# Performance work log

Measured on AMD Instinct MI355X. Metric: run time of the kernel, lower is better.

## Reference

```python
import jax, jax.numpy as jnp
import numpy as np

VOL = (32, 64, 64)          # 3D brain volume grid
B, N, D = 2, 4096, 1024     # batch, active voxels (seq_len), feature_dim
H, KNN = 16, 16             # num_heads, num_neighbors


def setup_inputs() -> dict:
    key = jax.random.key(0)
    k1, k2, k3, k4 = jax.random.split(key, 4)
    # boolean 3D mask with exactly N active voxels (so seq_len == #active)
    rng = np.random.default_rng(0)
    flat = np.zeros(int(np.prod(VOL)), dtype=bool)
    flat[rng.choice(flat.size, N, replace=False)] = True
    visual_cortex_mask = jnp.asarray(flat.reshape(VOL))
    x = jax.random.normal(k1, (B, N, D), dtype=jnp.float32)
    s = 1.0 / np.sqrt(D)
    Wq = jax.random.normal(k2, (D, D), dtype=jnp.float32) * s
    Wk = jax.random.normal(k3, (D, D), dtype=jnp.float32) * s
    Wv = jax.random.normal(k4, (D, D), dtype=jnp.float32) * s
    return {"x": x, "visual_cortex_mask": visual_cortex_mask,
            "Wq": Wq, "Wk": Wk, "Wv": Wv}


def reference(x, visual_cortex_mask, Wq, Wk, Wv):
    batch, seq_len, d = x.shape
    hd = d // H
    # --- kNN over active voxel coordinates (cdist + topk) ---
    flat = visual_cortex_mask.reshape(-1)
    (act,) = jnp.nonzero(flat, size=seq_len)  # flat indices of active voxels
    coords = jnp.stack(jnp.unravel_index(act, visual_cortex_mask.shape),
                       axis=1).astype(jnp.float32)           # [N, 3]
    sq = jnp.sum(coords * coords, axis=-1)                    # [N]
    d2 = sq[:, None] + sq[None, :] - 2.0 * (coords @ coords.T)  # squared dists
    _, nbr = jax.lax.top_k(-d2, KNN + 1)   # smallest distances first
    nbr = nbr[:, 1:]                       # drop self -> [N, KNN] positions
    # --- QKV projections (torch Linear: x @ W.T) ---
    q = (x @ Wq.T).reshape(batch, seq_len, H, hd)
    k = (x @ Wk.T).reshape(batch, seq_len, H, hd)
    v = (x @ Wv.T).reshape(batch, seq_len, H, hd)
    # --- gather-based sparse attention: each query attends only to its
    # KNN neighbors (exactly the block-mask semantics of the original) ---
    kn = k[:, nbr]   # [B, N, KNN, H, hd]
    vn = v[:, nbr]   # [B, N, KNN, H, hd]
    scale = 1.0 / np.sqrt(hd)
    scores = jnp.einsum('bnhd,bnkhd->bhnk', q, kn) * scale
    attn = jax.nn.softmax(scores, axis=-1)
    out = jnp.einsum('bhnk,bnkhd->bnhd', attn, vn).reshape(batch, seq_len, d)
    metric = k.mean(axis=2)  # key.mean over heads -> [B, N, hd]
    return out, metric
```

## Files before the change

kernel.cpp:

```cpp
#include <hip/hip_runtime.h>
#include <hip/hip_bf16.h>
#include <stdint.h>

#define BATCH 2
#define NPTS 4096
#define DMODEL 1024
#define NHEAD 16
#define HDIM 64
#define KNN 16
#define MASKN 131072
#define EBLK 128

typedef __attribute__((ext_vector_type(8))) short bf16x8;
typedef __attribute__((ext_vector_type(4))) float f32x4;

__device__ __forceinline__ float b2f(unsigned short u) {
    union { unsigned int i; float f; } c; c.i = ((unsigned int)u) << 16; return c.f;
}
__device__ __forceinline__ unsigned short f2b(float f) {
    unsigned int x = __float_as_uint(f);
    unsigned int r = (x + 0x7fffu + ((x >> 16) & 1u)) >> 16;
    return (unsigned short)r;
}
__device__ __forceinline__ unsigned int pack2f(float a, float b) {
    return (unsigned int)f2b(a) | ((unsigned int)f2b(b) << 16);
}
__device__ __forceinline__ void gload16(const unsigned short* g, unsigned short* l) {
    __builtin_amdgcn_global_load_lds((const __attribute__((address_space(1))) void*)g,
                                     (__attribute__((address_space(3))) void*)l, 16, 0, 0);
}

__global__ __launch_bounds__(256) void count8_kernel(const unsigned char* __restrict__ m8,
                                                     int* __restrict__ cnt8) {
    __shared__ int red[256];
    const int b = blockIdx.x, t = threadIdx.x;
    const uchar4 v = ((const uchar4*)m8)[b * 256 + t];
    red[t] = (v.x != 0) + (v.y != 0) + (v.z != 0) + (v.w != 0);
    __syncthreads();
    for (int off = 128; off >= 1; off >>= 1) {
        if (t < off) red[t] += red[t + off];
        __syncthreads();
    }
    if (t == 0) cnt8[b] = red[0];
}

__global__ __launch_bounds__(256) void count32_kernel(const unsigned char* __restrict__ m8,
                                                      const int* __restrict__ cnt8,
                                                      int* __restrict__ cnt32) {
    __shared__ int red[256];
    const int b = blockIdx.x, t = threadIdx.x;
    red[t] = (t < EBLK) ? cnt8[t] : 0;
    __syncthreads();
    for (int off = 128; off >= 1; off >>= 1) {
        if (t < off) red[t] += red[t + off];
        __syncthreads();
    }
    if (red[0] == NPTS) return;
    __syncthreads();
    const int4 v = ((const int4*)m8)[b * 256 + t];
    red[t] = (v.x != 0) + (v.y != 0) + (v.z != 0) + (v.w != 0);
    __syncthreads();
    for (int off = 128; off >= 1; off >>= 1) {
        if (t < off) red[t] += red[t + off];
        __syncthreads();
    }
    if (t == 0) cnt32[b] = red[0];
}

__global__ __launch_bounds__(256) void extract_kernel(const unsigned char* __restrict__ m8,
                                                      const int* __restrict__ cnt8,
                                                      const int* __restrict__ cnt32,
                                                      int* __restrict__ act) {
    __shared__ int sblk[EBLK];
    __shared__ int sthr[256];
    const int b = blockIdx.x, t = threadIdx.x;
    if (t < EBLK) sblk[t] = cnt8[t];
    __syncthreads();
    for (int off = 1; off < EBLK; off <<= 1) {
        int v = (t < EBLK && t >= off) ? sblk[t - off] : 0;
        __syncthreads();
        if (t < EBLK) sblk[t] += v;
        __syncthreads();
    }
    const bool bytes = (sblk[EBLK - 1] == NPTS);
    if (!bytes) {
        __syncthreads();
        if (t < EBLK) sblk[t] = cnt32[t];
        __syncthreads();
        for (int off = 1; off < EBLK; off <<= 1) {
            int v = (t < EBLK && t >= off) ? sblk[t - off] : 0;
            __syncthreads();
            if (t < EBLK) sblk[t] += v;
            __syncthreads();
        }
    }
    const int blkoff = (b == 0) ? 0 : sblk[b - 1];
    const int gbase = b * 1024 + t * 4;
    int f0, f1, f2, f3;
    if (bytes) {
        const uchar4 v = ((const uchar4*)m8)[b * 256 + t];
        f0 = v.x != 0; f1 = v.y != 0; f2 = v.z != 0; f3 = v.w != 0;
    } else {
        const int4 v = ((const int4*)m8)[b * 256 + t];
        f0 = v.x != 0; f1 = v.y != 0; f2 = v.z != 0; f3 = v.w != 0;
    }
    const int c = f0 + f1 + f2 + f3;
    sthr[t] = c;
    __syncthreads();
    for (int off = 1; off < 256; off <<= 1) {
        int v = (t >= off) ? sthr[t - off] : 0;
        __syncthreads();
        sthr[t] += v;
        __syncthreads();
    }
    int pos = blkoff + sthr[t] - c;
    if (f0) act[pos++] = gbase;
    if (f1) act[pos++] = gbase + 1;
    if (f2) act[pos++] = gbase + 2;
    if (f3) act[pos++] = gbase + 3;
}

__global__ __launch_bounds__(256) void knn_kernel(const int* __restrict__ act,
                                                  int* __restrict__ nbr) {
    __shared__ int act_s[NPTS];
    const int t = threadIdx.x;
    for (int i = t; i < NPTS; i += 256) act_s[i] = act[i];
    __syncthreads();
    const int q = blockIdx.x * 4 + (t >> 6);
    const int lane = t & 63;
    const int aq = act_s[q];
    const int qz = aq >> 12, qy = (aq >> 6) & 63, qx = aq & 63;
    int best[17];
    #pragma unroll
    for (int i = 0; i < 17; ++i) best[i] = 0x7FFFFFFF;
    for (int j = lane; j < NPTS; j += 64) {
        const int aj = act_s[j];
        const int dz = (aj >> 12) - qz;
        const int dy = ((aj >> 6) & 63) - qy;
        const int dx = (aj & 63) - qx;
        const int d2 = dz * dz + dy * dy + dx * dx;
        int p = (d2 << 12) | j;
        if (p < best[16]) {
            #pragma unroll
            for (int u = 0; u < 17; ++u) {
                const bool lt = p < best[u];
                const int tmp = best[u];
                best[u] = lt ? p : best[u];
                p = lt ? tmp : p;
            }
        }
    }
    int head = best[0];
    int keep = 0;
    #pragma unroll
    for (int r = 0; r < KNN + 1; ++r) {
        int m = head;
        #pragma unroll
        for (int off = 32; off >= 1; off >>= 1) m = min(m, __shfl_xor(m, off, 64));
        if (lane == r - 1) keep = m;
        const bool win = (head == m);
        #pragma unroll
        for (int u = 0; u < 16; ++u) if (win) best[u] = best[u + 1];
        if (win) best[16] = 0x7FFFFFFF;
        head = best[0];
    }
    if (lane < KNN) nbr[q * KNN + lane] = keep & 4095;
}

#define XN8 (BATCH * NPTS * DMODEL / 8)
#define WN8 (DMODEL * DMODEL / 8)
__global__ __launch_bounds__(256) void cast_all_kernel(
    const float* __restrict__ x, const float* __restrict__ wq,
    const float* __restrict__ wk, const float* __restrict__ wv,
    unsigned short* __restrict__ Xb, unsigned short* __restrict__ Wb) {
    const int i = blockIdx.x * 256 + threadIdx.x;
    const int total = XN8 + 3 * WN8;
    if (i >= total) return;
    const float* src;
    unsigned short* dst;
    if (i < XN8) {
        src = x + (size_t)i * 8;
        dst = Xb + (size_t)i * 8;
    } else {
        const int j = i - XN8;
        const int wsel = j >> 17;
        const int o = j & (WN8 - 1);
        src = ((wsel == 0) ? wq : (wsel == 1) ? wk : wv) + (size_t)o * 8;
        dst = Wb + ((size_t)wsel * WN8 + o) * 8;
    }
    const float4 a = ((const float4*)src)[0];
    const float4 b = ((const float4*)src)[1];
    uint4 w;
    w.x = pack2f(a.x, a.y); w.y = pack2f(a.z, a.w);
    w.z = pack2f(b.x, b.y); w.w = pack2f(b.z, b.w);
    *(uint4*)dst = w;
}

__global__ __launch_bounds__(256) void gemm_qkv_bf16(
    const unsigned short* __restrict__ Xb,
    const unsigned short* __restrict__ Wb,
    unsigned short* __restrict__ O0, unsigned short* __restrict__ O1, unsigned short* __restrict__ O2)
{
    const int K = DMODEL, N = DMODEL;
    const int bid = blockIdx.x;
    const int xcd = bid & 7;
    const int idx = bid >> 3;
    const int x   = xcd * 8 + (idx & 7);
    const int yz  = idx >> 3;
    const int y   = yz & 7;
    const int z   = yz >> 3;
    const unsigned short* W = Wb + (size_t)z * DMODEL * DMODEL;
    unsigned short* C = (z == 0) ? O0 : (z == 1) ? O1 : O2;
    __shared__ unsigned short As[2][128 * 32];
    __shared__ unsigned short Bs[2][128 * 32];
    const int tid = threadIdx.x;
    const int rowBase = x * 128;
    const int colBase = y * 128;
    const int lane = tid & 63, w = tid >> 6;
    const int wr = w >> 1, wc = w & 1;
    const int lr = lane & 15, kg = lane >> 4;

    f32x4 acc[4][4];
    const f32x4 zero = {0.f, 0.f, 0.f, 0.f};
    #pragma unroll
    for (int i = 0; i < 4; ++i)
        #pragma unroll
        for (int j = 0; j < 4; ++j) acc[i][j] = zero;

    const int srow4 = tid >> 2;
    const int xch = (tid & 3) ^ (srow4 & 3);
    const unsigned short* agp = &Xb[(size_t)(rowBase + srow4) * K + xch * 8];
    const unsigned short* bgp = &W[(size_t)(colBase + srow4) * K + xch * 8];
    unsigned short* a0[2] = { &As[0][w * 512], &As[1][w * 512] };
    unsigned short* a1[2] = { &As[0][2048 + w * 512], &As[1][2048 + w * 512] };
    unsigned short* b0[2] = { &Bs[0][w * 512], &Bs[1][w * 512] };
    unsigned short* b1[2] = { &Bs[0][2048 + w * 512], &Bs[1][2048 + w * 512] };

    #define STAGE(kt, bf) do { \
        gload16(agp + (kt) * 32,           a0[bf]); \
        gload16(agp + 64 * K + (kt) * 32,  a1[bf]); \
        gload16(bgp + (kt) * 32,           b0[bf]); \
        gload16(bgp + 64 * K + (kt) * 32,  b1[bf]); \
    } while (0)

    const int rchunk = (kg ^ (lr & 3)) * 8;

    #define COMPUTE(bf) do { \
        bf16x8 af[4], bfr[4]; \
        _Pragma("unroll") \
        for (int mi = 0; mi < 4; ++mi) \
            af[mi] = *(const bf16x8*)&As[bf][(wr * 64 + mi * 16 + lr) * 32 + rchunk]; \
        _Pragma("unroll") \
        for (int ni = 0; ni < 4; ++ni) \
            bfr[ni] = *(const bf16x8*)&Bs[bf][(wc * 64 + ni * 16 + lr) * 32 + rchunk]; \
        __builtin_amdgcn_s_setprio(1); \
        _Pragma("unroll") \
        for (int mi = 0; mi < 4; ++mi) \
            _Pragma("unroll") \
            for (int ni = 0; ni < 4; ++ni) \
                acc[mi][ni] = __builtin_amdgcn_mfma_f32_16x16x32_bf16(af[mi], bfr[ni], acc[mi][ni], 0, 0, 0); \
        __builtin_amdgcn_s_setprio(0); \
    } while (0)

    STAGE(0, 0);
    STAGE(1, 1);
    for (int kt = 0; kt < 30; ++kt) {
        const int bf = kt & 1;
        asm volatile("s_waitcnt vmcnt(4)" ::: "memory");
        __builtin_amdgcn_s_barrier();
        COMPUTE(bf);
        __builtin_amdgcn_s_barrier();
        STAGE(kt + 2, bf);
    }
    asm volatile("s_waitcnt vmcnt(4)" ::: "memory");
    __builtin_amdgcn_s_barrier();
    COMPUTE(0);
    __builtin_amdgcn_s_barrier();
    asm volatile("s_waitcnt vmcnt(0)" ::: "memory");
    __builtin_amdgcn_s_barrier();
    COMPUTE(1);
    #undef STAGE
    #undef COMPUTE

    #pragma unroll
    for (int mi = 0; mi < 4; ++mi)
        #pragma unroll
        for (int ni = 0; ni < 4; ++ni) {
            const int row0 = rowBase + wr * 64 + mi * 16 + kg * 4;
            const int col = colBase + wc * 64 + ni * 16 + lr;
            #pragma unroll
            for (int j = 0; j < 4; ++j)
                C[(size_t)(row0 + j) * N + col] = f2b(acc[mi][ni][j]);
        }
}

__device__ __forceinline__ void stage16(unsigned short* dst, const float* src) {
    const float4 a = ((const float4*)src)[0];
    const float4 b = ((const float4*)src)[1];
    const float4 c = ((const float4*)src)[2];
    const float4 d = ((const float4*)src)[3];
    uint4 w0, w1;
    w0.x = pack2f(a.x, a.y); w0.y = pack2f(a.z, a.w);
    w0.z = pack2f(b.x, b.y); w0.w = pack2f(b.z, b.w);
    w1.x = pack2f(c.x, c.y); w1.y = pack2f(c.z, c.w);
    w1.z = pack2f(d.x, d.y); w1.w = pack2f(d.z, d.w);
    ((uint4*)dst)[0] = w0;
    ((uint4*)dst)[1] = w1;
}

__global__ __launch_bounds__(256) void gemm_qkv_f32(
    const float* __restrict__ X,
    const float* __restrict__ W0, const float* __restrict__ W1, const float* __restrict__ W2,
    unsigned short* __restrict__ O0, unsigned short* __restrict__ O1, unsigned short* __restrict__ O2)
{
    const int K = DMODEL, N = DMODEL;
    const float* W = (blockIdx.z == 0) ? W0 : (blockIdx.z == 1) ? W1 : W2;
    unsigned short* C = (blockIdx.z == 0) ? O0 : (blockIdx.z == 1) ? O1 : O2;
    __shared__ unsigned short As[128 * 32];
    __shared__ unsigned short Bs[128 * 32];
    const int tid = threadIdx.x;
    const int rowBase = blockIdx.x * 128;
    const int colBase = blockIdx.y * 128;
    const int lane = tid & 63, w = tid >> 6;
    const int wr = w >> 1, wc = w & 1;
    const int lr = lane & 15, kg = lane >> 4;
    const int srow = tid >> 1;
    const int scol = (tid & 1) * 16;
    f32x4 acc[4][4];
    const f32x4 zero = {0.f, 0.f, 0.f, 0.f};
    #pragma unroll
    for (int i = 0; i < 4; ++i)
        #pragma unroll
        for (int j = 0; j < 4; ++j) acc[i][j] = zero;
    const float* Arow = &X[(size_t)(rowBase + srow) * K + scol];
    const float* Brow = &W[(size_t)(colBase + srow) * K + scol];
    unsigned short* Adst = &As[srow * 32 + scol];
    unsigned short* Bdst = &Bs[srow * 32 + scol];
    for (int kb = 0; kb < K; kb += 32) {
        __syncthreads();
        stage16(Adst, Arow + kb);
        stage16(Bdst, Brow + kb);
        __syncthreads();
        bf16x8 af[4], bfr[4];
        #pragma unroll
        for (int mi = 0; mi < 4; ++mi)
            af[mi] = *(const bf16x8*)&As[(wr * 64 + mi * 16 + lr) * 32 + kg * 8];
        #pragma unroll
        for (int ni = 0; ni < 4; ++ni)
            bfr[ni] = *(const bf16x8*)&Bs[(wc * 64 + ni * 16 + lr) * 32 + kg * 8];
        #pragma unroll
        for (int mi = 0; mi < 4; ++mi)
            #pragma unroll
            for (int ni = 0; ni < 4; ++ni)
                acc[mi][ni] = __builtin_amdgcn_mfma_f32_16x16x32_bf16(af[mi], bfr[ni], acc[mi][ni], 0, 0, 0);
    }
    #pragma unroll
    for (int mi = 0; mi < 4; ++mi)
        #pragma unroll
        for (int ni = 0; ni < 4; ++ni) {
            const int row0 = rowBase + wr * 64 + mi * 16 + kg * 4;
            const int col = colBase + wc * 64 + ni * 16 + lr;
            #pragma unroll
            for (int j = 0; j < 4; ++j)
                C[(size_t)(row0 + j) * N + col] = f2b(acc[mi][ni][j]);
        }
}

__global__ __launch_bounds__(256) void attn_kernel(
    const unsigned short* __restrict__ Q, const unsigned short* __restrict__ Kb,
    const unsigned short* __restrict__ Vb, const int* __restrict__ nbr,
    float* __restrict__ out)
{
    const int n = blockIdx.x;
    const int b = blockIdx.y;
    __shared__ unsigned short k_s[128][KNN][8];
    __shared__ unsigned short q_s[DMODEL];
    __shared__ float a_s[NHEAD][KNN];
    __shared__ int nb_s[KNN];
    const int tid = threadIdx.x;
    if (tid < KNN) nb_s[tid] = nbr[n * KNN + tid];
    *(int2*)&q_s[tid * 4] = *(const int2*)&Q[((size_t)b * NPTS + n) * DMODEL + tid * 4];
    __syncthreads();
    {
        const int kk = tid & 15;
        const int c0 = tid >> 4;
        const unsigned short* krow = &Kb[((size_t)b * NPTS + nb_s[kk]) * DMODEL];
        #pragma unroll
        for (int i = 0; i < 8; ++i) {
            const int c = c0 + 16 * i;
            *(uint4*)&k_s[c][kk][0] = *(const uint4*)&krow[c * 8];
        }
    }
    const int o = tid * 4;
    ushort4 vpre[KNN];
    #pragma unroll
    for (int k2 = 0; k2 < KNN; ++k2)
        vpre[k2] = *(const ushort4*)&Vb[((size_t)b * NPTS + nb_s[k2]) * DMODEL + o];
    __syncthreads();
    const int h = tid >> 4, kk = tid & 15;
    float s = 0.f;
    #pragma unroll
    for (int j = 0; j < 8; ++j) {
        const bf16x8 qq = *(const bf16x8*)&q_s[h * HDIM + j * 8];
        const bf16x8 kr = *(const bf16x8*)&k_s[h * 8 + j][kk][0];
        #pragma unroll
        for (int e = 0; e < 8; ++e)
            s += b2f((unsigned short)qq[e]) * b2f((unsigned short)kr[e]);
    }
    s *= 0.125f;
    float m = s;
    #pragma unroll
    for (int off = 8; off >= 1; off >>= 1) m = fmaxf(m, __shfl_xor(m, off, 16));
    const float e = __expf(s - m);
    float sum = e;
    #pragma unroll
    for (int off = 8; off >= 1; off >>= 1) sum += __shfl_xor(sum, off, 16);
    a_s[h][kk] = e / sum;
    __syncthreads();
    const int h2 = tid >> 4;
    float av0 = 0.f, av1 = 0.f, av2 = 0.f, av3 = 0.f;
    #pragma unroll
    for (int k2 = 0; k2 < KNN; ++k2) {
        const float a = a_s[h2][k2];
        av0 += a * b2f(vpre[k2].x); av1 += a * b2f(vpre[k2].y);
        av2 += a * b2f(vpre[k2].z); av3 += a * b2f(vpre[k2].w);
    }
    float4 r; r.x = av0; r.y = av1; r.z = av2; r.w = av3;
    *(float4*)&out[((size_t)b * NPTS + n) * DMODEL + o] = r;
}

__global__ __launch_bounds__(256) void metric_kernel(const unsigned short* __restrict__ Kb,
                                                     float* __restrict__ mout) {
    const int i = blockIdx.x * 256 + threadIdx.x;
    if (i >= BATCH * NPTS * HDIM) return;
    const int d = i & 63;
    const int bn = i >> 6;
    const unsigned short* kp = &Kb[(size_t)bn * DMODEL + d];
    float s = 0.f;
    #pragma unroll
    for (int hh = 0; hh < NHEAD; ++hh) s += b2f(kp[hh * HDIM]);
    mout[i] = s * 0.0625f;
}

extern "C" void kernel_launch(void* const* d_in, const int* in_sizes, int n_in,
                              void* d_out, int out_size, void* d_ws, size_t ws_size,
                              hipStream_t stream) {
    const float* x = (const float*)d_in[0];
    const unsigned char* mask = (const unsigned char*)d_in[1];
    const float* Wq = (const float*)d_in[2];
    const float* Wk = (const float*)d_in[3];
    const float* Wv = (const float*)d_in[4];
    float* out = (float*)d_out;
    char* ws = (char*)d_ws;

    const size_t QKV_BYTES = (size_t)BATCH * NPTS * DMODEL * 2;
    const size_t XB_BYTES  = (size_t)BATCH * NPTS * DMODEL * 2;
    const size_t WB_BYTES  = (size_t)3 * DMODEL * DMODEL * 2;
    unsigned short* qb = (unsigned short*)(ws);
    unsigned short* kb = (unsigned short*)(ws + QKV_BYTES);
    unsigned short* vb = (unsigned short*)(ws + 2 * QKV_BYTES);
    const size_t SMALL_BYTES = (size_t)NPTS * sizeof(int) * (1 + KNN) + 2 * EBLK * sizeof(int);
    const size_t need_base = 3 * QKV_BYTES + SMALL_BYTES;
    const size_t need_full = need_base + XB_BYTES + WB_BYTES;
    const bool full = (ws_size >= need_full);
    char* tail = ws + 3 * QKV_BYTES;
    unsigned short* Xb = (unsigned short*)tail;
    unsigned short* Wb = (unsigned short*)(tail + XB_BYTES);
    char* small = full ? (tail + XB_BYTES + WB_BYTES) : tail;
    int* act  = (int*)small;
    int* nbr  = (int*)(small + NPTS * sizeof(int));
    int* cnt8 = (int*)(small + NPTS * sizeof(int) * (1 + KNN));
    int* cnt32 = cnt8 + EBLK;
    if (ws_size < need_base) return;

    count8_kernel<<<EBLK, 256, 0, stream>>>(mask, cnt8);
    count32_kernel<<<EBLK, 256, 0, stream>>>(mask, cnt8, cnt32);
    extract_kernel<<<EBLK, 256, 0, stream>>>(mask, cnt8, cnt32, act);
    knn_kernel<<<1024, 256, 0, stream>>>(act, nbr);
    if (full) {
        const int castN = XN8 + 3 * WN8;
        cast_all_kernel<<<(castN + 255) / 256, 256, 0, stream>>>(x, Wq, Wk, Wv, Xb, Wb);
        gemm_qkv_bf16<<<dim3(1536), 256, 0, stream>>>(Xb, Wb, qb, kb, vb);
    } else {
        gemm_qkv_f32<<<dim3(64, 8, 3), 256, 0, stream>>>(x, Wq, Wk, Wv, qb, kb, vb);
    }
    attn_kernel<<<dim3(NPTS, BATCH), 256, 0, stream>>>(qb, kb, vb, nbr, out);
    metric_kernel<<<(BATCH * NPTS * HDIM + 255) / 256, 256, 0, stream>>>(kb, out + (size_t)BATCH * NPTS * DMODEL);
}
```

Before: 183.8 us.

## Fuse key-mean metric into attention kernel and remap block order

Removes the separate metric kernel and computes the per-point mean of K over heads inside the attention kernel, using a small shared-memory reduction across four thread groups. The launch becomes a 1D grid, and each block index is remapped so that consecutive blocks are spread 1024 points apart in the point order. This saves one kernel launch and one extra pass over K, in exchange for an added barrier and a K row read at the end of every attention block. The remapping changes which neighbor rows are resident in cache at the same time, which could help or hurt locality.

```diff
diff --git a/kernel.cpp b/kernel.cpp
--- a/kernel.cpp
+++ b/kernel.cpp
@@ -369,13 +369,16 @@
 __global__ __launch_bounds__(256) void attn_kernel(
     const unsigned short* __restrict__ Q, const unsigned short* __restrict__ Kb,
     const unsigned short* __restrict__ Vb, const int* __restrict__ nbr,
-    float* __restrict__ out)
+    float* __restrict__ out, float* __restrict__ mout)
 {
-    const int n = blockIdx.x;
-    const int b = blockIdx.y;
+    const int bid = blockIdx.x;
+    const int p = (bid & 7) * 1024 + (bid >> 3);
+    const int b = p >> 12;
+    const int n = p & 4095;
     __shared__ unsigned short k_s[128][KNN][8];
     __shared__ unsigned short q_s[DMODEL];
     __shared__ float a_s[NHEAD][KNN];
+    __shared__ float part_s[4][64];
     __shared__ int nb_s[KNN];
     const int tid = threadIdx.x;
     if (tid < KNN) nb_s[tid] = nbr[n * KNN + tid];
@@ -427,19 +430,19 @@
     }
     float4 r; r.x = av0; r.y = av1; r.z = av2; r.w = av3;
     *(float4*)&out[((size_t)b * NPTS + n) * DMODEL + o] = r;
-}
-
-__global__ __launch_bounds__(256) void metric_kernel(const unsigned short* __restrict__ Kb,
-                                                     float* __restrict__ mout) {
-    const int i = blockIdx.x * 256 + threadIdx.x;
-    if (i >= BATCH * NPTS * HDIM) return;
-    const int d = i & 63;
-    const int bn = i >> 6;
-    const unsigned short* kp = &Kb[(size_t)bn * DMODEL + d];
-    float s = 0.f;
-    #pragma unroll
-    for (int hh = 0; hh < NHEAD; ++hh) s += b2f(kp[hh * HDIM]);
-    mout[i] = s * 0.0625f;
+    {
+        const unsigned short* krow = &Kb[((size_t)b * NPTS + n) * DMODEL];
+        const int dd = tid & 63, grp = tid >> 6;
+        float ms = 0.f;
+        #pragma unroll
+        for (int hh = 0; hh < 4; ++hh)
+            ms += b2f(krow[(grp * 4 + hh) * HDIM + dd]);
+        part_s[grp][dd] = ms;
+        __syncthreads();
+        if (tid < 64)
+            mout[((size_t)b * NPTS + n) * HDIM + tid] =
+                (part_s[0][tid] + part_s[1][tid] + part_s[2][tid] + part_s[3][tid]) * 0.0625f;
+    }
 }
 
 extern "C" void kernel_launch(void* const* d_in, const int* in_sizes, int n_in,
@@ -484,6 +487,6 @@
     } else {
         gemm_qkv_f32<<<dim3(64, 8, 3), 256, 0, stream>>>(x, Wq, Wk, Wv, qb, kb, vb);
     }
-    attn_kernel<<<dim3(NPTS, BATCH), 256, 0, stream>>>(qb, kb, vb, nbr, out);
-    metric_kernel<<<(BATCH * NPTS * HDIM + 255) / 256, 256, 0, stream>>>(kb, out + (size_t)BATCH * NPTS * DMODEL);
-}
+    attn_kernel<<<dim3(BATCH * NPTS), 256, 0, stream>>>(qb, kb, vb, nbr, out,
+                                                        out + (size_t)BATCH * NPTS * DMODEL);
+}
```

Result: no change. 180.3 us (-1.9%).
